# Kernel optimization log

Measured on AMD Instinct MI355X. Metric: run time of the kernel, lower is better.

Reference implementation:

```python
import jax, jax.numpy as jnp
import numpy as np

B, N, D, H = 128, 256, 256, 256
N_POWER_ITERS = 5  # matches spectral_norm(n_power_iterations=5)


def setup_inputs() -> dict:
    key = jax.random.key(0)
    ks = jax.random.split(key, 8)
    w = lambda k, shape: jax.random.normal(k, shape, dtype=jnp.float32) * 0.05
    return {
        "x": jax.random.normal(ks[0], (B, N, D), dtype=jnp.float32),
        "Wq": w(ks[1], (H, D)), "bq": w(ks[2], (H,)),
        "Wk": w(ks[3], (H, D)), "bk": w(ks[4], (H,)),
        "Wv": w(ks[5], (D, D)), "bv": w(ks[6], (D,)),
        "u0": jax.random.normal(ks[7], (D,), dtype=jnp.float32),
    }


def _l2norm(v, eps=1e-12):
    return v / (jnp.linalg.norm(v) + eps)


def _spectral_normalize(W, u0):
    # torch spectral_norm: power iteration (no grad) to get u, v; sigma = u^T W v (with grad)
    u = _l2norm(u0)
    v = _l2norm(W.T @ u)
    def body(i, uv):
        u, v = uv
        v = _l2norm(W.T @ u)
        u = _l2norm(W @ v)
        return (u, v)
    u, v = jax.lax.fori_loop(0, N_POWER_ITERS, body, (u, v))
    u = jax.lax.stop_gradient(u)
    v = jax.lax.stop_gradient(v)
    sigma = u @ (W @ v)
    return W / sigma


def reference(x, Wq, bq, Wk, bk, Wv, bv, u0):
    # torch Linear: y = x @ W.T + b, W is [out, in]
    q = jnp.einsum('bnd,hd->bnh', x, Wq) + bq          # [B, N, H]
    k = jnp.einsum('bnd,hd->bnh', x, Wk) + bk          # [B, N, H]
    Wv_sn = _spectral_normalize(Wv, u0)
    vals = jnp.einsum('bnd,od->bno', x, Wv_sn) + bv    # [B, N, D]
    scores = jnp.einsum('bnh,bmh->bnm', q, k)          # [B, N, N]
    # track_grads=False -> eigenvals detached; stop_gradient input so eig has no tangent path
    ev = jnp.linalg.eigvals(jax.lax.stop_gradient(scores))  # complex [B, N]
    rho = jnp.max(jnp.abs(ev), axis=-1)[:, None, None]      # spectral radius [B,1,1]
    attention = scores / rho
    weighted = jnp.einsum('bnm,bmd->bnd', attention, vals)  # [B, N, D]
    return weighted, attention
```

## Files before the change

### kernel.cpp

```cpp
#include <hip/hip_runtime.h>
#include <hip/hip_bf16.h>


#define NB 128
#define MAT 65536
#define BIG 8388608LL

typedef __attribute__((ext_vector_type(4))) float floatx4;
typedef __attribute__((ext_vector_type(4))) float f4v;
typedef __attribute__((ext_vector_type(8))) short short8v;
typedef __attribute__((ext_vector_type(4))) short short4v;

__device__ __forceinline__ short f2bf(float x) {
  union { float f; unsigned u; } v; v.f = x;
  unsigned r = v.u + 0x7fff + ((v.u >> 16) & 1);
  return (short)(r >> 16);
}
__device__ __forceinline__ float bf2f(short h) {
  union { unsigned u; float f; } v; v.u = ((unsigned)(unsigned short)h) << 16; return v.f;
}

template<bool TB, bool BATCHED>
__global__ __launch_bounds__(256) void gemm_mfma(
    const float* __restrict__ A, const float* __restrict__ B, float* __restrict__ C,
    long long sA, long long sB, long long sC,
    const float* __restrict__ bias,
    const float* __restrict__ scale_ptr, int sstride, int smode,
    float* __restrict__ norm_out,
    float* __restrict__ att_out,
    const float* __restrict__ B2, const float* __restrict__ bias2, float* __restrict__ C2,
    const float* __restrict__ B3, float* __restrict__ C3,
    const float* __restrict__ bsc, const float* __restrict__ bsb)
{
  __shared__ short sAhi[128 * 32], sAlo[128 * 32];
  __shared__ short sBhi[128 * 40], sBlo[128 * 40];

  int bz, m0, n0;
  if constexpr (BATCHED) {
    int lin = blockIdx.x;
    int xcd = lin & 7;
    int s = lin >> 3;
    bz = xcd * 16 + (s >> 2);
    int tile = s & 3;
    m0 = (tile >> 1) * 128;
    n0 = (tile & 1) * 128;
  } else {
    bz = 0;
    m0 = blockIdx.y * 128;
    n0 = (blockIdx.x & 1) * 128;
    int sel = blockIdx.x >> 1;
    if (sel == 1) { B = B2; bias = bias2; C = C2; }
    else if (sel == 2) { B = B3; bias = nullptr; C = C3; }
  }
  A += (long long)bz * sA;
  B += (long long)bz * sB;
  C += (long long)bz * sC;

  const int t = threadIdx.x;
  const int lane = t & 63;
  const int wave = t >> 6;
  const int wm = wave >> 1, wn = wave & 1;
  const int q = lane >> 4, c16 = lane & 15;

  float alpha = 1.0f;
  if (smode == 1) alpha = 1.0f / scale_ptr[bz * sstride];
  else if (smode == 2) alpha = scale_ptr[bz * sstride];

  float rinv_att = alpha;
  const bool do_att = (att_out != nullptr) && (n0 == 0);

  float binv = 1.0f;
  if (bsc) binv = 1.0f / bsc[0];

  floatx4 acc[4][4];
  #pragma unroll
  for (int i = 0; i < 4; i++)
    #pragma unroll
    for (int j = 0; j < 4; j++)
      acc[i][j] = (floatx4){0.f, 0.f, 0.f, 0.f};

  for (int k0 = 0; k0 < 256; k0 += 32) {
    #pragma unroll
    for (int i = 0; i < 4; i++) {
      int f = t + i * 256;
      int row = f >> 3, c4 = f & 7;
      f4v v = *(const f4v*)(A + (long long)(m0 + row) * 256 + k0 + c4 * 4);
      if (do_att)
        *(f4v*)(att_out + (long long)bz * MAT + (long long)(m0 + row) * 256 + k0 + c4 * 4)
            = v * rinv_att;
      short4v h, l;
      #pragma unroll
      for (int e = 0; e < 4; e++) {
        short hh = f2bf(v[e]);
        h[e] = hh;
        l[e] = f2bf(v[e] - bf2f(hh));
      }
      *(short4v*)&sAhi[row * 32 + c4 * 4] = h;
      *(short4v*)&sAlo[row * 32 + c4 * 4] = l;
    }
    if constexpr (TB) {
      #pragma unroll
      for (int i = 0; i < 4; i++) {
        int f = t + i * 256;
        int row = f >> 3, c4 = f & 7;
        f4v v = *(const f4v*)(B + (long long)(n0 + row) * 256 + k0 + c4 * 4);
        short4v h, l;
        #pragma unroll
        for (int e = 0; e < 4; e++) {
          short hh = f2bf(v[e]);
          h[e] = hh;
          l[e] = f2bf(v[e] - bf2f(hh));
        }
        *(short4v*)&sBhi[row * 40 + c4 * 4] = h;
        *(short4v*)&sBlo[row * 40 + c4 * 4] = l;
      }
      __syncthreads();
    } else {
      __shared__ float sT[32 * 132];
      #pragma unroll
      for (int i = 0; i < 4; i++) {
        int f = t + i * 256;
        int kk = f >> 5, n4 = f & 31;
        f4v v = *(const f4v*)(B + (long long)(k0 + kk) * 256 + n0 + n4 * 4);
        if (bsb) {
          #pragma unroll
          for (int e = 0; e < 4; e++) v[e] = v[e] * binv + bsb[n0 + n4 * 4 + e];
        }
        *(f4v*)&sT[kk * 132 + n4 * 4] = v;
      }
      __syncthreads();
      int n = t & 127, kh = t >> 7;
      short8v h0, h1, l0, l1;
      #pragma unroll
      for (int j = 0; j < 8; j++) {
        float x0 = sT[(kh * 16 + j) * 132 + n];
        float x1 = sT[(kh * 16 + 8 + j) * 132 + n];
        short a0 = f2bf(x0), a1 = f2bf(x1);
        h0[j] = a0; l0[j] = f2bf(x0 - bf2f(a0));
        h1[j] = a1; l1[j] = f2bf(x1 - bf2f(a1));
      }
      *(short8v*)&sBhi[n * 40 + kh * 16] = h0;
      *(short8v*)&sBhi[n * 40 + kh * 16 + 8] = h1;
      *(short8v*)&sBlo[n * 40 + kh * 16] = l0;
      *(short8v*)&sBlo[n * 40 + kh * 16 + 8] = l1;
      __syncthreads();
    }

    short8v ah[4], al[4], bh[4], bl[4];
    #pragma unroll
    for (int fi = 0; fi < 4; fi++) {
      int r = wm * 64 + fi * 16 + c16;
      ah[fi] = *(short8v*)&sAhi[r * 32 + q * 8];
      al[fi] = *(short8v*)&sAlo[r * 32 + q * 8];
    }
    #pragma unroll
    for (int fj = 0; fj < 4; fj++) {
      int r = wn * 64 + fj * 16 + c16;
      bh[fj] = *(short8v*)&sBhi[r * 40 + q * 8];
      bl[fj] = *(short8v*)&sBlo[r * 40 + q * 8];
    }
    #pragma unroll
    for (int fi = 0; fi < 4; fi++)
      #pragma unroll
      for (int fj = 0; fj < 4; fj++) {
        acc[fi][fj] = __builtin_amdgcn_mfma_f32_16x16x32_bf16(al[fi], bh[fj], acc[fi][fj], 0, 0, 0);
        acc[fi][fj] = __builtin_amdgcn_mfma_f32_16x16x32_bf16(ah[fi], bl[fj], acc[fi][fj], 0, 0, 0);
        acc[fi][fj] = __builtin_amdgcn_mfma_f32_16x16x32_bf16(ah[fi], bh[fj], acc[fi][fj], 0, 0, 0);
      }
    __syncthreads();
  }

  float ssq = 0.f;
  #pragma unroll
  for (int fi = 0; fi < 4; fi++) {
    #pragma unroll
    for (int fj = 0; fj < 4; fj++) {
      int col = n0 + wn * 64 + fj * 16 + c16;
      float bb = bias ? bias[col] : 0.f;
      #pragma unroll
      for (int r = 0; r < 4; r++) {
        int row = m0 + wm * 64 + fi * 16 + q * 4 + r;
        float v = acc[fi][fj][r] * alpha + bb;
        C[(long long)row * 256 + col] = v;
        ssq += v * v;
      }
    }
  }

  if (norm_out) {
    float* red = (float*)sAhi;
    red[t] = ssq;
    __syncthreads();
    for (int off = 128; off > 0; off >>= 1) {
      if (t < off) red[t] += red[t + off];
      __syncthreads();
    }
    if (t == 0) {
      int tl = ((m0 >> 7) << 1) | (n0 >> 7);
      norm_out[bz * 4 + tl] = red[0];
    }
  }
}

__global__ __launch_bounds__(256) void split_w(
    const float* __restrict__ Wq, const float* __restrict__ Wk,
    const float* __restrict__ Wv, short* __restrict__ ws6)
{
  int gid = blockIdx.x * 256 + threadIdx.x;
  int m = gid >> 14;
  int off = (gid & 16383) * 4;
  const float* src = (m == 0) ? Wq : (m == 1) ? Wk : Wv;
  f4v v = *(const f4v*)(src + off);
  short4v h, l;
  #pragma unroll
  for (int e = 0; e < 4; e++) {
    short hh = f2bf(v[e]);
    h[e] = hh;
    l[e] = f2bf(v[e] - bf2f(hh));
  }
  *(short4v*)&ws6[(long long)(m * 2) * MAT + off] = h;
  *(short4v*)&ws6[(long long)(m * 2 + 1) * MAT + off] = l;
}

__global__ __launch_bounds__(256, 2) void proj3(
    const float* __restrict__ x, const short* __restrict__ wsp,
    const float* __restrict__ bq, const float* __restrict__ bk,
    short* __restrict__ qhi, short* __restrict__ qlo,
    short* __restrict__ khi, short* __restrict__ klo,
    float* __restrict__ vals)
{
  __shared__ short sAhi[128 * 40], sAlo[128 * 40];

  const int n0 = (blockIdx.x & 1) * 128;
  const int grp = blockIdx.x >> 1;
  const int m0 = blockIdx.y * 128;

  const int t = threadIdx.x;
  const int lane = t & 63;
  const int wave = t >> 6;
  const int wm = wave >> 1, wn = wave & 1;
  const int q = lane >> 4, c16 = lane & 15;

  if (grp == 0) {
    floatx4 acc0[4][4], acc1[4][4];
    #pragma unroll
    for (int i = 0; i < 4; i++)
      #pragma unroll
      for (int j = 0; j < 4; j++) {
        acc0[i][j] = (floatx4){0.f, 0.f, 0.f, 0.f};
        acc1[i][j] = (floatx4){0.f, 0.f, 0.f, 0.f};
      }

    for (int k0 = 0; k0 < 256; k0 += 32) {
      if (k0) __syncthreads();
      #pragma unroll
      for (int i = 0; i < 4; i++) {
        int f = t + i * 256;
        int row = f >> 3, c4 = f & 7;
        f4v v = *(const f4v*)(x + (long long)(m0 + row) * 256 + k0 + c4 * 4);
        short4v h, l;
        #pragma unroll
        for (int e = 0; e < 4; e++) {
          short hh = f2bf(v[e]);
          h[e] = hh;
          l[e] = f2bf(v[e] - bf2f(hh));
        }
        *(short4v*)&sAhi[row * 40 + c4 * 4] = h;
        *(short4v*)&sAlo[row * 40 + c4 * 4] = l;
      }
      __syncthreads();

      short8v ah[4], al[4];
      #pragma unroll
      for (int fi = 0; fi < 4; fi++) {
        int r = wm * 64 + fi * 16 + c16;
        ah[fi] = *(short8v*)&sAhi[r * 40 + q * 8];
        al[fi] = *(short8v*)&sAlo[r * 40 + q * 8];
      }
      {
        short8v bh[4], bl[4];
        #pragma unroll
        for (int fj = 0; fj < 4; fj++) {
          long long r = (long long)(n0 + wn * 64 + fj * 16 + c16) * 256 + k0 + q * 8;
          bh[fj] = *(const short8v*)(wsp + r);
          bl[fj] = *(const short8v*)(wsp + MAT + r);
        }
        #pragma unroll
        for (int fi = 0; fi < 4; fi++)
          #pragma unroll
          for (int fj = 0; fj < 4; fj++) {
            acc0[fi][fj] = __builtin_amdgcn_mfma_f32_16x16x32_bf16(al[fi], bh[fj], acc0[fi][fj], 0, 0, 0);
            acc0[fi][fj] = __builtin_amdgcn_mfma_f32_16x16x32_bf16(ah[fi], bl[fj], acc0[fi][fj], 0, 0, 0);
            acc0[fi][fj] = __builtin_amdgcn_mfma_f32_16x16x32_bf16(ah[fi], bh[fj], acc0[fi][fj], 0, 0, 0);
          }
      }
      {
        short8v bh[4], bl[4];
        #pragma unroll
        for (int fj = 0; fj < 4; fj++) {
          long long r = (long long)(n0 + wn * 64 + fj * 16 + c16) * 256 + k0 + q * 8;
          bh[fj] = *(const short8v*)(wsp + 2LL * MAT + r);
          bl[fj] = *(const short8v*)(wsp + 3LL * MAT + r);
        }
        #pragma unroll
        for (int fi = 0; fi < 4; fi++)
          #pragma unroll
          for (int fj = 0; fj < 4; fj++) {
            acc1[fi][fj] = __builtin_amdgcn_mfma_f32_16x16x32_bf16(al[fi], bh[fj], acc1[fi][fj], 0, 0, 0);
            acc1[fi][fj] = __builtin_amdgcn_mfma_f32_16x16x32_bf16(ah[fi], bl[fj], acc1[fi][fj], 0, 0, 0);
            acc1[fi][fj] = __builtin_amdgcn_mfma_f32_16x16x32_bf16(ah[fi], bh[fj], acc1[fi][fj], 0, 0, 0);
          }
      }
    }

    #pragma unroll
    for (int fi = 0; fi < 4; fi++)
      #pragma unroll
      for (int fj = 0; fj < 4; fj++) {
        int col = n0 + wn * 64 + fj * 16 + c16;
        float bbq = bq[col], bbk = bk[col];
        #pragma unroll
        for (int r = 0; r < 4; r++) {
          long long row = m0 + wm * 64 + fi * 16 + q * 4 + r;
          float vq = acc0[fi][fj][r] + bbq;
          float vk = acc1[fi][fj][r] + bbk;
          short hq = f2bf(vq), hk = f2bf(vk);
          qhi[row * 256 + col] = hq;
          qlo[row * 256 + col] = f2bf(vq - bf2f(hq));
          khi[row * 256 + col] = hk;
          klo[row * 256 + col] = f2bf(vk - bf2f(hk));
        }
      }
  } else {
    floatx4 acc[4][4];
    #pragma unroll
    for (int i = 0; i < 4; i++)
      #pragma unroll
      for (int j = 0; j < 4; j++)
        acc[i][j] = (floatx4){0.f, 0.f, 0.f, 0.f};

    for (int k0 = 0; k0 < 256; k0 += 32) {
      if (k0) __syncthreads();
      #pragma unroll
      for (int i = 0; i < 4; i++) {
        int f = t + i * 256;
        int row = f >> 3, c4 = f & 7;
        f4v v = *(const f4v*)(x + (long long)(m0 + row) * 256 + k0 + c4 * 4);
        short4v h, l;
        #pragma unroll
        for (int e = 0; e < 4; e++) {
          short hh = f2bf(v[e]);
          h[e] = hh;
          l[e] = f2bf(v[e] - bf2f(hh));
        }
        *(short4v*)&sAhi[row * 40 + c4 * 4] = h;
        *(short4v*)&sAlo[row * 40 + c4 * 4] = l;
      }
      __syncthreads();

      short8v ah[4], al[4], bh[4], bl[4];
      #pragma unroll
      for (int fi = 0; fi < 4; fi++) {
        int r = wm * 64 + fi * 16 + c16;
        ah[fi] = *(short8v*)&sAhi[r * 40 + q * 8];
        al[fi] = *(short8v*)&sAlo[r * 40 + q * 8];
      }
      #pragma unroll
      for (int fj = 0; fj < 4; fj++) {
        long long r = (long long)(n0 + wn * 64 + fj * 16 + c16) * 256 + k0 + q * 8;
        bh[fj] = *(const short8v*)(wsp + 4LL * MAT + r);
        bl[fj] = *(const short8v*)(wsp + 5LL * MAT + r);
      }
      #pragma unroll
      for (int fi = 0; fi < 4; fi++)
        #pragma unroll
        for (int fj = 0; fj < 4; fj++) {
          acc[fi][fj] = __builtin_amdgcn_mfma_f32_16x16x32_bf16(al[fi], bh[fj], acc[fi][fj], 0, 0, 0);
          acc[fi][fj] = __builtin_amdgcn_mfma_f32_16x16x32_bf16(ah[fi], bl[fj], acc[fi][fj], 0, 0, 0);
          acc[fi][fj] = __builtin_amdgcn_mfma_f32_16x16x32_bf16(ah[fi], bh[fj], acc[fi][fj], 0, 0, 0);
        }
    }

    #pragma unroll
    for (int fi = 0; fi < 4; fi++)
      #pragma unroll
      for (int fj = 0; fj < 4; fj++) {
        int col = n0 + wn * 64 + fj * 16 + c16;
        #pragma unroll
        for (int r = 0; r < 4; r++) {
          long long row = m0 + wm * 64 + fi * 16 + q * 4 + r;
          vals[row * 256 + col] = acc[fi][fj][r];
        }
      }
  }
}

__global__ __launch_bounds__(256) void scores_direct(
    const short* __restrict__ qhi, const short* __restrict__ qlo,
    const short* __restrict__ khi, const short* __restrict__ klo,
    float* __restrict__ S, float* __restrict__ norm_out)
{
  __shared__ float red[256];

  const int lin = blockIdx.x;
  const int xcd = lin & 7, s = lin >> 3;
  const int bz = xcd * 16 + (s >> 2);
  const int tile = s & 3;
  const int m0 = (tile >> 1) * 128, n0 = (tile & 1) * 128;

  const int t = threadIdx.x;
  const int lane = t & 63;
  const int wave = t >> 6;
  const int wm = wave >> 1, wn = wave & 1;
  const int q = lane >> 4, c16 = lane & 15;

  floatx4 acc[4][4];
  #pragma unroll
  for (int i = 0; i < 4; i++)
    #pragma unroll
    for (int j = 0; j < 4; j++)
      acc[i][j] = (floatx4){0.f, 0.f, 0.f, 0.f};

  const long long arow = (long long)(bz * 256 + m0 + wm * 64) * 256;
  const long long brow = (long long)(bz * 256 + n0 + wn * 64) * 256;

  for (int k0 = 0; k0 < 256; k0 += 32) {
    short8v ah[4], al[4], bh[4], bl[4];
    #pragma unroll
    for (int fi = 0; fi < 4; fi++) {
      long long r = arow + (long long)(fi * 16 + c16) * 256 + k0 + q * 8;
      ah[fi] = *(const short8v*)(qhi + r);
      al[fi] = *(const short8v*)(qlo + r);
    }
    #pragma unroll
    for (int fj = 0; fj < 4; fj++) {
      long long r = brow + (long long)(fj * 16 + c16) * 256 + k0 + q * 8;
      bh[fj] = *(const short8v*)(khi + r);
      bl[fj] = *(const short8v*)(klo + r);
    }
    #pragma unroll
    for (int fi = 0; fi < 4; fi++)
      #pragma unroll
      for (int fj = 0; fj < 4; fj++) {
        acc[fi][fj] = __builtin_amdgcn_mfma_f32_16x16x32_bf16(al[fi], bh[fj], acc[fi][fj], 0, 0, 0);
        acc[fi][fj] = __builtin_amdgcn_mfma_f32_16x16x32_bf16(ah[fi], bl[fj], acc[fi][fj], 0, 0, 0);
        acc[fi][fj] = __builtin_amdgcn_mfma_f32_16x16x32_bf16(ah[fi], bh[fj], acc[fi][fj], 0, 0, 0);
      }
  }

  float* C = S + (long long)bz * MAT;
  float ssq = 0.f;
  #pragma unroll
  for (int fi = 0; fi < 4; fi++)
    #pragma unroll
    for (int fj = 0; fj < 4; fj++) {
      int col = n0 + wn * 64 + fj * 16 + c16;
      #pragma unroll
      for (int r = 0; r < 4; r++) {
        int row = m0 + wm * 64 + fi * 16 + q * 4 + r;
        float v = acc[fi][fj][r];
        C[(long long)row * 256 + col] = v;
        ssq += v * v;
      }
    }

  red[t] = ssq;
  __syncthreads();
  for (int off = 128; off > 0; off >>= 1) {
    if (t < off) red[t] += red[t + off];
    __syncthreads();
  }
  if (t == 0) norm_out[bz * 4 + tile] = red[0];
}

__device__ __forceinline__ void chain_epilogue(
    short* LB, float* red, floatx4 (&acc)[4][4], float alpha,
    int m0, int n0, int wm, int wn, int q, int c16, int t,
    short* __restrict__ Mout,
    float* __restrict__ nout, int bz, int tile, bool write_out)
{
  __syncthreads();
  float ssq = 0.f;
  #pragma unroll
  for (int fi = 0; fi < 4; fi++)
    #pragma unroll
    for (int fj = 0; fj < 4; fj++) {
      int lcol = wn * 64 + fj * 16 + c16;
      #pragma unroll
      for (int r = 0; r < 4; r++) {
        int lrow = wm * 64 + fi * 16 + q * 4 + r;
        float v = acc[fi][fj][r] * alpha;
        ssq += v * v;
        if (write_out) LB[lrow * 128 + lcol] = f2bf(v);
      }
    }

  if (write_out) {
    __syncthreads();
    int lr = t >> 1, off = (t & 1) * 64;
    #pragma unroll
    for (int jc = 0; jc < 8; jc++)
      *(short8v*)(Mout + (long long)(m0 + lr) * 256 + n0 + off + jc * 8)
          = *(const short8v*)&LB[lr * 128 + off + jc * 8];
  }

  red[t] = ssq;
  __syncthreads();
  for (int off2 = 128; off2 > 0; off2 >>= 1) {
    if (t < off2) red[t] += red[t + off2];
    __syncthreads();
  }
  if (t == 0) nout[bz * 4 + tile] = red[0];
}

__global__ __launch_bounds__(256) void sq_f32bf(
    const float* __restrict__ S, short* __restrict__ Mo,
    const float* __restrict__ nprev, float* __restrict__ nout)
{
  __shared__ short SM[18432];
  __shared__ float sT[32 * 132];
  __shared__ float red[256];
  short* sAhi = SM;
  short* sAlo = SM + 4096;
  short* sBhi = SM + 8192;
  short* sBlo = SM + 13312;

  int lin = blockIdx.x;
  int xcd = lin & 7, s = lin >> 3;
  int bz = xcd * 16 + (s >> 2);
  int tile = s & 3;
  int m0 = (tile >> 1) * 128, n0 = (tile & 1) * 128;
  const float* A = S + (long long)bz * MAT;

  const int t = threadIdx.x;
  const int lane = t & 63;
  const int wave = t >> 6;
  const int wm = wave >> 1, wn = wave & 1;
  const int q = lane >> 4, c16 = lane & 15;

  floatx4 acc[4][4];
  #pragma unroll
  for (int i = 0; i < 4; i++)
    #pragma unroll
    for (int j = 0; j < 4; j++)
      acc[i][j] = (floatx4){0.f, 0.f, 0.f, 0.f};

  for (int k0 = 0; k0 < 256; k0 += 32) {
    #pragma unroll
    for (int i = 0; i < 4; i++) {
      int f = t + i * 256;
      int row = f >> 3, c4 = f & 7;
      f4v v = *(const f4v*)(A + (long long)(m0 + row) * 256 + k0 + c4 * 4);
      short4v h, l;
      #pragma unroll
      for (int e = 0; e < 4; e++) {
        short hh = f2bf(v[e]);
        h[e] = hh;
        l[e] = f2bf(v[e] - bf2f(hh));
      }
      *(short4v*)&sAhi[row * 32 + c4 * 4] = h;
      *(short4v*)&sAlo[row * 32 + c4 * 4] = l;
    }
    #pragma unroll
    for (int i = 0; i < 4; i++) {
      int f = t + i * 256;
      int kk = f >> 5, n4 = f & 31;
      f4v v = *(const f4v*)(A + (long long)(k0 + kk) * 256 + n0 + n4 * 4);
      *(f4v*)&sT[kk * 132 + n4 * 4] = v;
    }
    __syncthreads();
    {
      int n = t & 127, kh = t >> 7;
      short8v h0, h1, l0, l1;
      #pragma unroll
      for (int j = 0; j < 8; j++) {
        float x0 = sT[(kh * 16 + j) * 132 + n];
        float x1 = sT[(kh * 16 + 8 + j) * 132 + n];
        short a0 = f2bf(x0), a1 = f2bf(x1);
        h0[j] = a0; l0[j] = f2bf(x0 - bf2f(a0));
        h1[j] = a1; l1[j] = f2bf(x1 - bf2f(a1));
      }
      *(short8v*)&sBhi[n * 40 + kh * 16] = h0;
      *(short8v*)&sBhi[n * 40 + kh * 16 + 8] = h1;
      *(short8v*)&sBlo[n * 40 + kh * 16] = l0;
      *(short8v*)&sBlo[n * 40 + kh * 16 + 8] = l1;
    }
    __syncthreads();

    short8v ah[4], al[4], bh[4], bl[4];
    #pragma unroll
    for (int fi = 0; fi < 4; fi++) {
      int r = wm * 64 + fi * 16 + c16;
      ah[fi] = *(short8v*)&sAhi[r * 32 + q * 8];
      al[fi] = *(short8v*)&sAlo[r * 32 + q * 8];
    }
    #pragma unroll
    for (int fj = 0; fj < 4; fj++) {
      int r = wn * 64 + fj * 16 + c16;
      bh[fj] = *(short8v*)&sBhi[r * 40 + q * 8];
      bl[fj] = *(short8v*)&sBlo[r * 40 + q * 8];
    }
    #pragma unroll
    for (int fi = 0; fi < 4; fi++)
      #pragma unroll
      for (int fj = 0; fj < 4; fj++) {
        acc[fi][fj] = __builtin_amdgcn_mfma_f32_16x16x32_bf16(al[fi], bh[fj], acc[fi][fj], 0, 0, 0);
        acc[fi][fj] = __builtin_amdgcn_mfma_f32_16x16x32_bf16(ah[fi], bl[fj], acc[fi][fj], 0, 0, 0);
        acc[fi][fj] = __builtin_amdgcn_mfma_f32_16x16x32_bf16(ah[fi], bh[fj], acc[fi][fj], 0, 0, 0);
      }
    __syncthreads();
  }

  const float* p = nprev + bz * 4;
  float alpha = 1.0f / (p[0] + p[1] + p[2] + p[3]);
  chain_epilogue(SM, red, acc, alpha, m0, n0, wm, wn, q, c16, t,
                 Mo + (long long)bz * MAT, nout, bz, tile, true);
}

template<bool WRITE_OUT>
__global__ __launch_bounds__(256) void sq_bf(
    const short* __restrict__ Mi, short* __restrict__ Mo,
    const float* __restrict__ nprev, float* __restrict__ nout)
{
  __shared__ short SMEM[16384];
  __shared__ float red[256];
  short* Bs = SMEM;

  int lin = blockIdx.x;
  int xcd = lin & 7, s = lin >> 3;
  int bz = xcd * 16 + (s >> 2);
  int tile = s & 3;
  int m0 = (tile >> 1) * 128, n0 = (tile & 1) * 128;

  const short* A = Mi + (long long)bz * MAT;

  const int t = threadIdx.x;
  const int lane = t & 63;
  const int wave = t >> 6;
  const int wm = wave >> 1, wn = wave & 1;
  const int q = lane >> 4, c16 = lane & 15;
  const int g = t >> 5, cc = t & 31;

  floatx4 acc[4][4];
  #pragma unroll
  for (int i = 0; i < 4; i++)
    #pragma unroll
    for (int j = 0; j < 4; j++)
      acc[i][j] = (floatx4){0.f, 0.f, 0.f, 0.f};

  for (int k0 = 0; k0 < 256; k0 += 32) {
    __syncthreads();
    short4v r0 = *(const short4v*)(A + (long long)(k0 + g * 4 + 0) * 256 + n0 + cc * 4);
    short4v r1 = *(const short4v*)(A + (long long)(k0 + g * 4 + 1) * 256 + n0 + cc * 4);
    short4v r2 = *(const short4v*)(A + (long long)(k0 + g * 4 + 2) * 256 + n0 + cc * 4);
    short4v r3 = *(const short4v*)(A + (long long)(k0 + g * 4 + 3) * 256 + n0 + cc * 4);
    #pragma unroll
    for (int j = 0; j < 4; j++) {
      short4v w4 = (short4v){r0[j], r1[j], r2[j], r3[j]};
      *(short4v*)&Bs[(cc * 4 + j) * 36 + g * 4] = w4;
    }
    __syncthreads();

    short8v a[4], b[4];
    #pragma unroll
    for (int fi = 0; fi < 4; fi++)
      a[fi] = *(const short8v*)(A + (long long)(m0 + wm * 64 + fi * 16 + c16) * 256 + k0 + q * 8);
    #pragma unroll
    for (int fj = 0; fj < 4; fj++) {
      int n = wn * 64 + fj * 16 + c16;
      short4v lo = *(const short4v*)&Bs[n * 36 + q * 8];
      short4v hi = *(const short4v*)&Bs[n * 36 + q * 8 + 4];
      b[fj] = __builtin_shufflevector(lo, hi, 0, 1, 2, 3, 4, 5, 6, 7);
    }
    #pragma unroll
    for (int fi = 0; fi < 4; fi++)
      #pragma unroll
      for (int fj = 0; fj < 4; fj++)
        acc[fi][fj] = __builtin_amdgcn_mfma_f32_16x16x32_bf16(a[fi], b[fj], acc[fi][fj], 0, 0, 0);
  }

  const float* p = nprev + bz * 4;
  float alpha = 1.0f / (p[0] + p[1] + p[2] + p[3]);
  chain_epilogue(SMEM, red, acc, alpha, m0, n0, wm, wn, q, c16, t,
                 WRITE_OUT ? Mo + (long long)bz * MAT : nullptr,
                 nout, bz, tile, WRITE_OUT);
}

__global__ __launch_bounds__(128) void rho_finalize(
    const float* __restrict__ partials, float* __restrict__ rho_inv)
{
  int bz = threadIdx.x;
  float a2 = 0.f, w = 1.0f;
  #pragma unroll
  for (int i2 = 0; i2 <= 12; i2++) {
    const float* p = partials + i2 * 512 + bz * 4;
    a2 += w * 0.5f * logf(p[0] + p[1] + p[2] + p[3]);
    w *= 0.5f;
  }
  rho_inv[bz] = expf(-a2);
}

__device__ __forceinline__ float bsum1024(float x, float* red, int t)
{
  red[t] = x; __syncthreads();
  for (int off = 512; off > 0; off >>= 1) {
    if (t < off) red[t] += red[t + off];
    __syncthreads();
  }
  float r = red[0];
  __syncthreads();
  return r;
}

__global__ __launch_bounds__(1024) void sigma_kernel(
    const float* __restrict__ W, const float* __restrict__ u0, float* __restrict__ sigma)
{
  __shared__ short Wl[65536];
  __shared__ float u[256], v[256], red[1024];
  int t = threadIdx.x;
  int r = t & 255, seg = t >> 8;
  const float eps = 1e-12f;

  #pragma unroll
  for (int i = 0; i < 16; i++) {
    int idx = (i * 1024 + t) * 4;
    f4v w = *(const f4v*)(W + idx);
    short4v h;
    #pragma unroll
    for (int e = 0; e < 4; e++) h[e] = f2bf(w[e]);
    *(short4v*)&Wl[idx] = h;
  }

  float x = (t < 256) ? u0[t] : 0.f;
  float nrm = sqrtf(bsum1024(x * x, red, t));
  if (t < 256) u[t] = x / (nrm + eps);
  __syncthreads();

  for (int it = 0; it < 5; it++) {
    float sv = 0.f;
    #pragma unroll 8
    for (int j = 0; j < 64; j++) {
      int h = seg * 64 + j;
      sv = fmaf(bf2f(Wl[h * 256 + r]), u[h], sv);
    }
    red[t] = sv; __syncthreads();
    float vr = 0.f;
    if (t < 256) vr = red[t] + red[256 + t] + red[512 + t] + red[768 + t];
    __syncthreads();
    nrm = sqrtf(bsum1024(t < 256 ? vr * vr : 0.f, red, t));
    if (t < 256) v[t] = vr / (nrm + eps);
    __syncthreads();
    if (it < 4) {
      float su = 0.f;
      #pragma unroll
      for (int j = 0; j < 16; j++) {
        short4v w4 = *(const short4v*)&Wl[r * 256 + seg * 64 + j * 4];
        const float* vv = &v[seg * 64 + j * 4];
        su += bf2f(w4[0]) * vv[0] + bf2f(w4[1]) * vv[1]
            + bf2f(w4[2]) * vv[2] + bf2f(w4[3]) * vv[3];
      }
      red[t] = su; __syncthreads();
      float ur = 0.f;
      if (t < 256) ur = red[t] + red[256 + t] + red[512 + t] + red[768 + t];
      __syncthreads();
      nrm = sqrtf(bsum1024(t < 256 ? ur * ur : 0.f, red, t));
      if (t < 256) u[t] = ur / (nrm + eps);
      __syncthreads();
    }
  }

  float z = 0.f;
  #pragma unroll
  for (int j = 0; j < 16; j++) {
    f4v w = *(const f4v*)(W + r * 256 + seg * 64 + j * 4);
    const float* vv = &v[seg * 64 + j * 4];
    z += w[0] * vv[0] + w[1] * vv[1] + w[2] * vv[2] + w[3] * vv[3];
  }
  red[t] = z; __syncthreads();
  float zr = 0.f;
  if (t < 256) zr = red[t] + red[256 + t] + red[512 + t] + red[768 + t];
  __syncthreads();
  float zz = bsum1024(t < 256 ? zr * zr : 0.f, red, t);
  if (t == 0) sigma[0] = sqrtf(zz);
}

extern "C" void kernel_launch(void* const* d_in, const int* in_sizes, int n_in,
                              void* d_out, int out_size, void* d_ws, size_t ws_size,
                              hipStream_t stream)
{
  const float* x  = (const float*)d_in[0];
  const float* Wq = (const float*)d_in[1];
  const float* bq = (const float*)d_in[2];
  const float* Wk = (const float*)d_in[3];
  const float* bk = (const float*)d_in[4];
  const float* Wv = (const float*)d_in[5];
  const float* bv = (const float*)d_in[6];
  const float* u0 = (const float*)d_in[7];

  float* out  = (float*)d_out;
  float* out0 = out;
  float* out1 = out + BIG;
  short* out0s = (short*)out0;
  short* out1s = (short*)out1;

  short* qhi = out0s;
  short* qlo = out0s + 32768LL * 256;
  short* khi = out1s;
  short* klo = out1s + 32768LL * 256;

  float* ws         = (float*)d_ws;
  float* scores_buf = ws;
  float* vals_buf   = ws + BIG;
  float* partials   = ws + 2 * BIG;
  float* sigma      = partials + 13 * 512;
  float* rho_inv    = sigma + 4;
  short* wsplit     = (short*)ws;

  dim3 blk(256);

  split_w<<<dim3(192, 1, 1), blk, 0, stream>>>(Wq, Wk, Wv, wsplit);

  proj3<<<dim3(4, 256, 1), blk, 0, stream>>>(
      x, wsplit, bq, bk, qhi, qlo, khi, klo, vals_buf);

  scores_direct<<<dim3(512, 1, 1), blk, 0, stream>>>(
      qhi, qlo, khi, klo, scores_buf, partials);

  sigma_kernel<<<1, dim3(1024), 0, stream>>>(Wv, u0, sigma);

  sq_f32bf<<<dim3(512, 1, 1), blk, 0, stream>>>(scores_buf, out0s, partials, partials + 512);

  const short* cin = out0s;
  for (int i = 0; i < 10; i++) {
    short* cout = (i & 1) ? out0s : out1s;
    sq_bf<true><<<dim3(512, 1, 1), blk, 0, stream>>>(cin, cout,
        partials + (1 + i) * 512, partials + (2 + i) * 512);
    cin = cout;
  }
  sq_bf<false><<<dim3(512, 1, 1), blk, 0, stream>>>(cin, nullptr,
      partials + 11 * 512, partials + 12 * 512);

  rho_finalize<<<1, dim3(128), 0, stream>>>(partials, rho_inv);

  gemm_mfma<false, true><<<dim3(512, 1, 1), blk, 0, stream>>>(
      scores_buf, vals_buf, out0, MAT, MAT, MAT, nullptr, rho_inv, 1, 2, nullptr,
      out1, nullptr, nullptr, nullptr, nullptr, nullptr, sigma, bv);
}
```

Before: 529.6 us.

## Stage weight and QK tiles in LDS, split projection grid, prefetch in matrix-square kernel

```diff
diff --git a/kernel.cpp b/kernel.cpp
--- a/kernel.cpp
+++ b/kernel.cpp
@@ -222,18 +222,27 @@
   *(short4v*)&ws6[(long long)(m * 2 + 1) * MAT + off] = l;
 }
 
-__global__ __launch_bounds__(256, 2) void proj3(
+__global__ __launch_bounds__(256) void proj_qkv(
     const float* __restrict__ x, const short* __restrict__ wsp,
     const float* __restrict__ bq, const float* __restrict__ bk,
     short* __restrict__ qhi, short* __restrict__ qlo,
     short* __restrict__ khi, short* __restrict__ klo,
     float* __restrict__ vals)
 {
-  __shared__ short sAhi[128 * 40], sAlo[128 * 40];
-
-  const int n0 = (blockIdx.x & 1) * 128;
-  const int grp = blockIdx.x >> 1;
-  const int m0 = blockIdx.y * 128;
+  __shared__ short sAhi[128 * 32], sAlo[128 * 32];
+  __shared__ short sBhi[128 * 40], sBlo[128 * 40];
+
+  const int lin = blockIdx.x;
+  const int xcd = lin & 7;
+  const int idx = lin >> 3;
+  const int mloc = idx / 6;
+  const int s6 = idx - mloc * 6;
+  const int m0 = (xcd * 32 + mloc) * 128;
+  const int sel = s6 >> 1;
+  const int n0 = (s6 & 1) * 128;
+
+  const short* wb_hi = wsp + (long long)(sel * 2) * MAT;
+  const short* wb_lo = wsp + (long long)(sel * 2 + 1) * MAT;
 
   const int t = threadIdx.x;
   const int lane = t & 63;
@@ -241,146 +250,83 @@
   const int wm = wave >> 1, wn = wave & 1;
   const int q = lane >> 4, c16 = lane & 15;
 
-  if (grp == 0) {
-    floatx4 acc0[4][4], acc1[4][4];
-    #pragma unroll
-    for (int i = 0; i < 4; i++)
-      #pragma unroll
-      for (int j = 0; j < 4; j++) {
-        acc0[i][j] = (floatx4){0.f, 0.f, 0.f, 0.f};
-        acc1[i][j] = (floatx4){0.f, 0.f, 0.f, 0.f};
-      }
-
-    for (int k0 = 0; k0 < 256; k0 += 32) {
-      if (k0) __syncthreads();
-      #pragma unroll
-      for (int i = 0; i < 4; i++) {
-        int f = t + i * 256;
-        int row = f >> 3, c4 = f & 7;
-        f4v v = *(const f4v*)(x + (long long)(m0 + row) * 256 + k0 + c4 * 4);
-        short4v h, l;
-        #pragma unroll
-        for (int e = 0; e < 4; e++) {
-          short hh = f2bf(v[e]);
-          h[e] = hh;
-          l[e] = f2bf(v[e] - bf2f(hh));
-        }
-        *(short4v*)&sAhi[row * 40 + c4 * 4] = h;
-        *(short4v*)&sAlo[row * 40 + c4 * 4] = l;
-      }
-      __syncthreads();
-
-      short8v ah[4], al[4];
-      #pragma unroll
-      for (int fi = 0; fi < 4; fi++) {
-        int r = wm * 64 + fi * 16 + c16;
-        ah[fi] = *(short8v*)&sAhi[r * 40 + q * 8];
-        al[fi] = *(short8v*)&sAlo[r * 40 + q * 8];
-      }
-      {
-        short8v bh[4], bl[4];
-        #pragma unroll
-        for (int fj = 0; fj < 4; fj++) {
-          long long r = (long long)(n0 + wn * 64 + fj * 16 + c16) * 256 + k0 + q * 8;
-          bh[fj] = *(const short8v*)(wsp + r);
-          bl[fj] = *(const short8v*)(wsp + MAT + r);
-        }
-        #pragma unroll
-        for (int fi = 0; fi < 4; fi++)
-          #pragma unroll
-          for (int fj = 0; fj < 4; fj++) {
-            acc0[fi][fj] = __builtin_amdgcn_mfma_f32_16x16x32_bf16(al[fi], bh[fj], acc0[fi][fj], 0, 0, 0);
-            acc0[fi][fj] = __builtin_amdgcn_mfma_f32_16x16x32_bf16(ah[fi], bl[fj], acc0[fi][fj], 0, 0, 0);
-            acc0[fi][fj] = __builtin_amdgcn_mfma_f32_16x16x32_bf16(ah[fi], bh[fj], acc0[fi][fj], 0, 0, 0);
-          }
-      }
-      {
-        short8v bh[4], bl[4];
-        #pragma unroll
-        for (int fj = 0; fj < 4; fj++) {
-          long long r = (long long)(n0 + wn * 64 + fj * 16 + c16) * 256 + k0 + q * 8;
-          bh[fj] = *(const short8v*)(wsp + 2LL * MAT + r);
-          bl[fj] = *(const short8v*)(wsp + 3LL * MAT + r);
-        }
-        #pragma unroll
-        for (int fi = 0; fi < 4; fi++)
-          #pragma unroll
-          for (int fj = 0; fj < 4; fj++) {
-            acc1[fi][fj] = __builtin_amdgcn_mfma_f32_16x16x32_bf16(al[fi], bh[fj], acc1[fi][fj], 0, 0, 0);
-            acc1[fi][fj] = __builtin_amdgcn_mfma_f32_16x16x32_bf16(ah[fi], bl[fj], acc1[fi][fj], 0, 0, 0);
-            acc1[fi][fj] = __builtin_amdgcn_mfma_f32_16x16x32_bf16(ah[fi], bh[fj], acc1[fi][fj], 0, 0, 0);
-          }
-      }
-    }
-
+  floatx4 acc[4][4];
+  #pragma unroll
+  for (int i = 0; i < 4; i++)
+    #pragma unroll
+    for (int j = 0; j < 4; j++)
+      acc[i][j] = (floatx4){0.f, 0.f, 0.f, 0.f};
+
+  for (int k0 = 0; k0 < 256; k0 += 32) {
+    #pragma unroll
+    for (int i = 0; i < 4; i++) {
+      int f = t + i * 256;
+      int row = f >> 3, c4 = f & 7;
+      f4v v = *(const f4v*)(x + (long long)(m0 + row) * 256 + k0 + c4 * 4);
+      short4v h, l;
+      #pragma unroll
+      for (int e = 0; e < 4; e++) {
+        short hh = f2bf(v[e]);
+        h[e] = hh;
+        l[e] = f2bf(v[e] - bf2f(hh));
+      }
+      *(short4v*)&sAhi[row * 32 + c4 * 4] = h;
+      *(short4v*)&sAlo[row * 32 + c4 * 4] = l;
+    }
+    #pragma unroll
+    for (int i = 0; i < 2; i++) {
+      int chunk = t + i * 256;
+      int row = chunk >> 2, c8 = chunk & 3;
+      long long gr = (long long)(n0 + row) * 256 + k0 + c8 * 8;
+      *(short8v*)&sBhi[row * 40 + c8 * 8] = *(const short8v*)(wb_hi + gr);
+      *(short8v*)&sBlo[row * 40 + c8 * 8] = *(const short8v*)(wb_lo + gr);
+    }
+    __syncthreads();
+
+    short8v ah[4], al[4], bh[4], bl[4];
+    #pragma unroll
+    for (int fi = 0; fi < 4; fi++) {
+      int r = wm * 64 + fi * 16 + c16;
+      ah[fi] = *(short8v*)&sAhi[r * 32 + q * 8];
+      al[fi] = *(short8v*)&sAlo[r * 32 + q * 8];
+    }
+    #pragma unroll
+    for (int fj = 0; fj < 4; fj++) {
+      int r = wn * 64 + fj * 16 + c16;
+      bh[fj] = *(short8v*)&sBhi[r * 40 + q * 8];
+      bl[fj] = *(short8v*)&sBlo[r * 40 + q * 8];
+    }
+    #pragma unroll
+    for (int fi = 0; fi < 4; fi++)
+      #pragma unroll
+      for (int fj = 0; fj < 4; fj++) {
+        acc[fi][fj] = __builtin_amdgcn_mfma_f32_16x16x32_bf16(al[fi], bh[fj], acc[fi][fj], 0, 0, 0);
+        acc[fi][fj] = __builtin_amdgcn_mfma_f32_16x16x32_bf16(ah[fi], bl[fj], acc[fi][fj], 0, 0, 0);
+        acc[fi][fj] = __builtin_amdgcn_mfma_f32_16x16x32_bf16(ah[fi], bh[fj], acc[fi][fj], 0, 0, 0);
+      }
+    __syncthreads();
+  }
+
+  if (sel < 2) {
+    short* ohi = sel ? khi : qhi;
+    short* olo = sel ? klo : qlo;
+    const float* bb = sel ? bk : bq;
     #pragma unroll
     for (int fi = 0; fi < 4; fi++)
       #pragma unroll
       for (int fj = 0; fj < 4; fj++) {
         int col = n0 + wn * 64 + fj * 16 + c16;
-        float bbq = bq[col], bbk = bk[col];
+        float b = bb[col];
         #pragma unroll
         for (int r = 0; r < 4; r++) {
           long long row = m0 + wm * 64 + fi * 16 + q * 4 + r;
-          float vq = acc0[fi][fj][r] + bbq;
-          float vk = acc1[fi][fj][r] + bbk;
-          short hq = f2bf(vq), hk = f2bf(vk);
-          qhi[row * 256 + col] = hq;
-          qlo[row * 256 + col] = f2bf(vq - bf2f(hq));
-          khi[row * 256 + col] = hk;
-          klo[row * 256 + col] = f2bf(vk - bf2f(hk));
+          float v = acc[fi][fj][r] + b;
+          short h = f2bf(v);
+          ohi[row * 256 + col] = h;
+          olo[row * 256 + col] = f2bf(v - bf2f(h));
         }
       }
   } else {
-    floatx4 acc[4][4];
-    #pragma unroll
-    for (int i = 0; i < 4; i++)
-      #pragma unroll
-      for (int j = 0; j < 4; j++)
-        acc[i][j] = (floatx4){0.f, 0.f, 0.f, 0.f};
-
-    for (int k0 = 0; k0 < 256; k0 += 32) {
-      if (k0) __syncthreads();
-      #pragma unroll
-      for (int i = 0; i < 4; i++) {
-        int f = t + i * 256;
-        int row = f >> 3, c4 = f & 7;
-        f4v v = *(const f4v*)(x + (long long)(m0 + row) * 256 + k0 + c4 * 4);
-        short4v h, l;
-        #pragma unroll
-        for (int e = 0; e < 4; e++) {
-          short hh = f2bf(v[e]);
-          h[e] = hh;
-          l[e] = f2bf(v[e] - bf2f(hh));
-        }
-        *(short4v*)&sAhi[row * 40 + c4 * 4] = h;
-        *(short4v*)&sAlo[row * 40 + c4 * 4] = l;
-      }
-      __syncthreads();
-
-      short8v ah[4], al[4], bh[4], bl[4];
-      #pragma unroll
-      for (int fi = 0; fi < 4; fi++) {
-        int r = wm * 64 + fi * 16 + c16;
-        ah[fi] = *(short8v*)&sAhi[r * 40 + q * 8];
-        al[fi] = *(short8v*)&sAlo[r * 40 + q * 8];
-      }
-      #pragma unroll
-      for (int fj = 0; fj < 4; fj++) {
-        long long r = (long long)(n0 + wn * 64 + fj * 16 + c16) * 256 + k0 + q * 8;
-        bh[fj] = *(const short8v*)(wsp + 4LL * MAT + r);
-        bl[fj] = *(const short8v*)(wsp + 5LL * MAT + r);
-      }
-      #pragma unroll
-      for (int fi = 0; fi < 4; fi++)
-        #pragma unroll
-        for (int fj = 0; fj < 4; fj++) {
-          acc[fi][fj] = __builtin_amdgcn_mfma_f32_16x16x32_bf16(al[fi], bh[fj], acc[fi][fj], 0, 0, 0);
-          acc[fi][fj] = __builtin_amdgcn_mfma_f32_16x16x32_bf16(ah[fi], bl[fj], acc[fi][fj], 0, 0, 0);
-          acc[fi][fj] = __builtin_amdgcn_mfma_f32_16x16x32_bf16(ah[fi], bh[fj], acc[fi][fj], 0, 0, 0);
-        }
-    }
-
     #pragma unroll
     for (int fi = 0; fi < 4; fi++)
       #pragma unroll
@@ -395,11 +341,13 @@
   }
 }
 
-__global__ __launch_bounds__(256) void scores_direct(
+__global__ __launch_bounds__(256) void scores_st(
     const short* __restrict__ qhi, const short* __restrict__ qlo,
     const short* __restrict__ khi, const short* __restrict__ klo,
     float* __restrict__ S, float* __restrict__ norm_out)
 {
+  __shared__ short sAhi[128 * 32], sAlo[128 * 32];
+  __shared__ short sBhi[128 * 40], sBlo[128 * 40];
   __shared__ float red[256];
 
   const int lin = blockIdx.x;
@@ -421,22 +369,35 @@
     for (int j = 0; j < 4; j++)
       acc[i][j] = (floatx4){0.f, 0.f, 0.f, 0.f};
 
-  const long long arow = (long long)(bz * 256 + m0 + wm * 64) * 256;
-  const long long brow = (long long)(bz * 256 + n0 + wn * 64) * 256;
+  const long long abase = (long long)(bz * 256 + m0) * 256;
+  const long long bbase = (long long)(bz * 256 + n0) * 256;
 
   for (int k0 = 0; k0 < 256; k0 += 32) {
+    #pragma unroll
+    for (int i = 0; i < 2; i++) {
+      int chunk = t + i * 256;
+      int row = chunk >> 2, c8 = chunk & 3;
+      long long ga = abase + (long long)row * 256 + k0 + c8 * 8;
+      long long gb = bbase + (long long)row * 256 + k0 + c8 * 8;
+      *(short8v*)&sAhi[row * 32 + c8 * 8] = *(const short8v*)(qhi + ga);
+      *(short8v*)&sAlo[row * 32 + c8 * 8] = *(const short8v*)(qlo + ga);
+      *(short8v*)&sBhi[row * 40 + c8 * 8] = *(const short8v*)(khi + gb);
+      *(short8v*)&sBlo[row * 40 + c8 * 8] = *(const short8v*)(klo + gb);
+    }
+    __syncthreads();
+
     short8v ah[4], al[4], bh[4], bl[4];
     #pragma unroll
     for (int fi = 0; fi < 4; fi++) {
-      long long r = arow + (long long)(fi * 16 + c16) * 256 + k0 + q * 8;
-      ah[fi] = *(const short8v*)(qhi + r);
-      al[fi] = *(const short8v*)(qlo + r);
+      int r = wm * 64 + fi * 16 + c16;
+      ah[fi] = *(short8v*)&sAhi[r * 32 + q * 8];
+      al[fi] = *(short8v*)&sAlo[r * 32 + q * 8];
     }
     #pragma unroll
     for (int fj = 0; fj < 4; fj++) {
-      long long r = brow + (long long)(fj * 16 + c16) * 256 + k0 + q * 8;
-      bh[fj] = *(const short8v*)(khi + r);
-      bl[fj] = *(const short8v*)(klo + r);
+      int r = wn * 64 + fj * 16 + c16;
+      bh[fj] = *(short8v*)&sBhi[r * 40 + q * 8];
+      bl[fj] = *(short8v*)&sBlo[r * 40 + q * 8];
     }
     #pragma unroll
     for (int fi = 0; fi < 4; fi++)
@@ -446,6 +407,7 @@
         acc[fi][fj] = __builtin_amdgcn_mfma_f32_16x16x32_bf16(ah[fi], bl[fj], acc[fi][fj], 0, 0, 0);
         acc[fi][fj] = __builtin_amdgcn_mfma_f32_16x16x32_bf16(ah[fi], bh[fj], acc[fi][fj], 0, 0, 0);
       }
+    __syncthreads();
   }
 
   float* C = S + (long long)bz * MAT;
@@ -648,18 +610,27 @@
     for (int j = 0; j < 4; j++)
       acc[i][j] = (floatx4){0.f, 0.f, 0.f, 0.f};
 
+  short4v r0 = *(const short4v*)(A + (long long)(g * 4 + 0) * 256 + n0 + cc * 4);
+  short4v r1 = *(const short4v*)(A + (long long)(g * 4 + 1) * 256 + n0 + cc * 4);
+  short4v r2 = *(const short4v*)(A + (long long)(g * 4 + 2) * 256 + n0 + cc * 4);
+  short4v r3 = *(const short4v*)(A + (long long)(g * 4 + 3) * 256 + n0 + cc * 4);
+
   for (int k0 = 0; k0 < 256; k0 += 32) {
     __syncthreads();
-    short4v r0 = *(const short4v*)(A + (long long)(k0 + g * 4 + 0) * 256 + n0 + cc * 4);
-    short4v r1 = *(const short4v*)(A + (long long)(k0 + g * 4 + 1) * 256 + n0 + cc * 4);
-    short4v r2 = *(const short4v*)(A + (long long)(k0 + g * 4 + 2) * 256 + n0 + cc * 4);
-    short4v r3 = *(const short4v*)(A + (long long)(k0 + g * 4 + 3) * 256 + n0 + cc * 4);
     #pragma unroll
     for (int j = 0; j < 4; j++) {
       short4v w4 = (short4v){r0[j], r1[j], r2[j], r3[j]};
       *(short4v*)&Bs[(cc * 4 + j) * 36 + g * 4] = w4;
     }
     __syncthreads();
+
+    if (k0 < 224) {
+      int kn = k0 + 32;
+      r0 = *(const short4v*)(A + (long long)(kn + g * 4 + 0) * 256 + n0 + cc * 4);
+      r1 = *(const short4v*)(A + (long long)(kn + g * 4 + 1) * 256 + n0 + cc * 4);
+      r2 = *(const short4v*)(A + (long long)(kn + g * 4 + 2) * 256 + n0 + cc * 4);
+      r3 = *(const short4v*)(A + (long long)(kn + g * 4 + 3) * 256 + n0 + cc * 4);
+    }
 
     short8v a[4], b[4];
     #pragma unroll
@@ -820,10 +791,10 @@
 
   split_w<<<dim3(192, 1, 1), blk, 0, stream>>>(Wq, Wk, Wv, wsplit);
 
-  proj3<<<dim3(4, 256, 1), blk, 0, stream>>>(
+  proj_qkv<<<dim3(1536, 1, 1), blk, 0, stream>>>(
       x, wsplit, bq, bk, qhi, qlo, khi, klo, vals_buf);
 
-  scores_direct<<<dim3(512, 1, 1), blk, 0, stream>>>(
+  scores_st<<<dim3(512, 1, 1), blk, 0, stream>>>(
       qhi, qlo, khi, klo, scores_buf, partials);
 
   sigma_kernel<<<1, dim3(1024), 0, stream>>>(Wv, u0, sigma);
```

Result: faster. 484.2 us (-8.6%).
